# Kernel tuning notes

Measured on AMD Instinct MI355X. Metric: run time of the kernel, lower is better.

Reference implementation:

```python
import jax, jax.numpy as jnp
import numpy as np

S = 7  # output_size
B, C, HF, WF = 8, 256, 160, 160
N = 128
IMG = 640


def setup_inputs() -> dict:
    key = jax.random.key(0)
    k1, k2, k3, k4 = jax.random.split(key, 4)
    feature_map = jax.random.normal(k1, (B, C, HF, WF), jnp.float32)
    # boxes in image-pixel coordinates (the module divides by image_size itself)
    pts = jax.random.uniform(k2, (B, N, 2, 2), jnp.float32, 0.0, float(IMG))
    lo = jnp.min(pts, axis=2)  # (x1, y1)
    hi = jnp.max(pts, axis=2)  # (x2, y2)
    bboxes = jnp.concatenate([lo, hi], axis=-1)  # [B, N, 4]
    proj_w = jax.random.normal(k3, (C, C), jnp.float32) * (1.0 / np.sqrt(C))
    proj_b = jax.random.normal(k4, (C,), jnp.float32) * 0.01
    return {"feature_map": feature_map, "bboxes": bboxes,
            "proj_w": proj_w, "proj_b": proj_b,
            "image_h": IMG, "image_w": IMG}


def _forward(feature_map, bboxes, proj_w, proj_b, image_h, image_w):
    Bb, Cc, Hf, Wf = feature_map.shape
    # 1x1 conv projection
    f = jnp.einsum('bchw,oc->bohw', feature_map, proj_w) + proj_b[None, :, None, None]
    # scale boxes from image coords to feature coords, then integer clip (as in torch code)
    sx = float(Wf) / float(image_w)
    sy = float(Hf) / float(image_h)
    x1 = jnp.clip(jnp.floor(bboxes[..., 0] * sx).astype(jnp.int32), 0, Wf - 1)
    y1 = jnp.clip(jnp.floor(bboxes[..., 1] * sy).astype(jnp.int32), 0, Hf - 1)
    x2 = jnp.clip(jnp.floor(bboxes[..., 2] * sx).astype(jnp.int32), x1 + 1, Wf)
    y2 = jnp.clip(jnp.floor(bboxes[..., 3] * sy).astype(jnp.int32), y1 + 1, Hf)
    Lx = x2 - x1  # [B, N], >= 1 by construction
    Ly = y2 - y1
    i = jnp.arange(S, dtype=jnp.int32)
    # adaptive_avg_pool2d bin edges: start=floor(i*L/S), end=ceil((i+1)*L/S)
    rs = y1[..., None] + (i * Ly[..., None]) // S            # [B, N, S]
    re = y1[..., None] + ((i + 1) * Ly[..., None] + S - 1) // S
    cs = x1[..., None] + (i * Lx[..., None]) // S
    ce = x1[..., None] + ((i + 1) * Lx[..., None] + S - 1) // S
    # summed-area table (zero-padded): I[b,c,y,x] = sum of f[b,c,:y,:x]
    I = jnp.cumsum(jnp.cumsum(f, axis=2), axis=3)
    I = jnp.pad(I, ((0, 0), (0, 0), (1, 0), (1, 0)))

    def per_batch(Ib, rs_b, re_b, cs_b, ce_b):
        # Ib: [C, Hf+1, Wf+1]; index arrays: [N, S]
        tl = Ib[:, rs_b[:, :, None], cs_b[:, None, :]]
        tr = Ib[:, rs_b[:, :, None], ce_b[:, None, :]]
        bl = Ib[:, re_b[:, :, None], cs_b[:, None, :]]
        br = Ib[:, re_b[:, :, None], ce_b[:, None, :]]
        return br - tr - bl + tl  # [C, N, S, S]

    sums = jax.vmap(per_batch)(I, rs, re, cs, ce)  # [B, C, N, S, S]
    counts = ((re - rs)[..., :, None] * (ce - cs)[..., None, :]).astype(f.dtype)  # [B, N, S, S]
    region_features = jnp.transpose(sums, (0, 2, 1, 3, 4)) / counts[:, :, None, :, :]
    # area in raw bbox units, as in the original code
    area_ratios = (bboxes[..., 2] - bboxes[..., 0]) * (bboxes[..., 3] - bboxes[..., 1])
    return region_features, area_ratios


def reference(feature_map, bboxes, proj_w, proj_b, image_h, image_w):
    return _forward(feature_map, bboxes, proj_w, proj_b, image_h, image_w)
```

## Files before the change

### kernel.cpp

```cpp
#include <hip/hip_runtime.h>
#include <hip/hip_bf16.h>

#define BB 8
#define NN 128
#define CC 256
#define HFD 160
#define WFD 160
#define SS 7
#define REGION_OUT_ELEMS (8*128*256*49)

typedef short short8 __attribute__((ext_vector_type(8)));
typedef float f32x4  __attribute__((ext_vector_type(4)));

__global__ __launch_bounds__(256) void k0_convert_w(const float* __restrict__ W,
                                                    __hip_bfloat16* __restrict__ Wb) {
    int o = blockIdx.x;
    int c = threadIdx.x;
    Wb[o * CC + c] = __float2bfloat16(W[o * CC + c]);
}

__global__ __launch_bounds__(256) void k1_rowsum_transpose(const float* __restrict__ fm,
                                                           float* __restrict__ R) {
    int bid = blockIdx.x;
    int cq  = bid & 3;
    int bh  = bid >> 2;
    int h   = bh % HFD;
    int b   = bh / HFD;
    int c0  = cq * 64;
    int t   = threadIdx.x;

    __shared__ float tile[64][161];
    __shared__ float segsum[64][5];

    #pragma unroll
    for (int it = 0; it < 10; ++it) {
        int vid = it * 256 + t;
        int c_l = vid / 40;
        int wq  = vid - c_l * 40;
        f32x4 v = __builtin_nontemporal_load(
            (const f32x4*)(fm + (((size_t)(b * CC + c0 + c_l)) * HFD + h) * WFD + wq * 4));
        tile[c_l][wq * 4 + 0] = v.x;
        tile[c_l][wq * 4 + 1] = v.y;
        tile[c_l][wq * 4 + 2] = v.z;
        tile[c_l][wq * 4 + 3] = v.w;
    }
    __syncthreads();

    int seg = t >> 6;
    int row = t & 63;
    {
        float s = 0.f;
        int w0 = seg * 40;
        #pragma unroll 8
        for (int k = 0; k < 40; ++k) {
            s += tile[row][w0 + k];
            tile[row][w0 + k] = s;
        }
        segsum[row][seg] = s;
    }
    __syncthreads();
    if (t < 64) {
        float a0 = segsum[t][0];
        float a1 = a0 + segsum[t][1];
        float a2 = a1 + segsum[t][2];
        segsum[t][1] = a0;
        segsum[t][2] = a1;
        segsum[t][3] = a2;
    }
    __syncthreads();
    if (seg > 0) {
        float off = segsum[row][seg];
        int w0 = seg * 40;
        #pragma unroll 8
        for (int k = 0; k < 40; ++k) tile[row][w0 + k] += off;
    }
    __syncthreads();

    size_t obase = (((size_t)b * HFD + h) * WFD) * CC + c0;
    #pragma unroll
    for (int it = 0; it < 10; ++it) {
        int vid = it * 256 + t;
        int w   = vid >> 4;
        int cg  = vid & 15;
        float4 o;
        o.x = tile[cg * 4 + 0][w];
        o.y = tile[cg * 4 + 1][w];
        o.z = tile[cg * 4 + 2][w];
        o.w = tile[cg * 4 + 3][w];
        *(float4*)(R + obase + (size_t)w * CC + cg * 4) = o;
    }
}

__global__ __launch_bounds__(256) void k2_colsum(float* __restrict__ I) {
    int w = blockIdx.x % WFD;
    int b = blockIdx.x / WFD;
    int c = threadIdx.x;
    float* p = I + (((size_t)b * HFD) * WFD + w) * CC + c;
    const size_t stride = (size_t)WFD * CC;
    float s = 0.f;
    #pragma unroll 16
    for (int h = 0; h < HFD; ++h) {
        float v = p[(size_t)h * stride];
        s += v;
        p[(size_t)h * stride] = s;
    }
}

__global__ __launch_bounds__(512) void k3a_gather(
        const float* __restrict__ I, const float* __restrict__ bboxes,
        const int* __restrict__ ih_p, const int* __restrict__ iw_p,
        __hip_bfloat16* __restrict__ Pm, float* __restrict__ out) {
    int bn = blockIdx.x;
    int b  = bn >> 7;
    int t  = threadIdx.x;
    int c  = t & 255;
    int half = t >> 8;

    float bx1 = bboxes[bn * 4 + 0];
    float by1 = bboxes[bn * 4 + 1];
    float bx2 = bboxes[bn * 4 + 2];
    float by2 = bboxes[bn * 4 + 3];
    float sx = (float)WFD / (float)iw_p[0];
    float sy = (float)HFD / (float)ih_p[0];

    int x1 = min(max((int)floorf(bx1 * sx), 0), WFD - 1);
    int y1 = min(max((int)floorf(by1 * sy), 0), HFD - 1);
    int x2 = min(max((int)floorf(bx2 * sx), x1 + 1), WFD);
    int y2 = min(max((int)floorf(by2 * sy), y1 + 1), HFD);
    int Lx = x2 - x1, Ly = y2 - y1;

    int rs[SS], re[SS], cs[SS], ce[SS];
    #pragma unroll
    for (int i = 0; i < SS; ++i) {
        rs[i] = y1 + (i * Ly) / SS;
        re[i] = y1 + ((i + 1) * Ly + SS - 1) / SS;
        cs[i] = x1 + (i * Lx) / SS;
        ce[i] = x1 + ((i + 1) * Lx + SS - 1) / SS;
    }

    const size_t Ib = (size_t)b * HFD * WFD * CC;
    __hip_bfloat16* pmb = Pm + (size_t)bn * 64 * CC;

#define GATHER_CELL(cell)                                                        \
    {                                                                            \
        const int i_ = (cell) / SS, j_ = (cell) % SS;                            \
        int r0 = rs[i_] - 1, r1 = re[i_] - 1;                                    \
        int c0 = cs[j_] - 1, c1 = ce[j_] - 1;                                    \
        float br = I[Ib + ((size_t)(r1 * WFD + c1)) * CC + c];                   \
        float tr = (r0 >= 0) ? I[Ib + ((size_t)(r0 * WFD + c1)) * CC + c] : 0.f; \
        float bl = (c0 >= 0) ? I[Ib + ((size_t)(r1 * WFD + c0)) * CC + c] : 0.f; \
        float tl = (r0 >= 0 && c0 >= 0) ? I[Ib + ((size_t)(r0 * WFD + c0)) * CC + c] : 0.f; \
        float cnt = (float)(re[i_] - rs[i_]) * (float)(ce[j_] - cs[j_]);         \
        pmb[(cell) * CC + c] = __float2bfloat16((br - tr - bl + tl) / cnt);      \
    }

    if (half == 0) {
        #pragma unroll
        for (int k = 0; k < 25; ++k) GATHER_CELL(k);
    } else {
        #pragma unroll
        for (int k = 25; k < 49; ++k) GATHER_CELL(k);
        __hip_bfloat16 z = __float2bfloat16(0.f);
        #pragma unroll
        for (int r = 49; r < 64; ++r) pmb[r * CC + c] = z;
    }
#undef GATHER_CELL

    if (t == 0) {
        __builtin_nontemporal_store((bx2 - bx1) * (by2 - by1), &out[REGION_OUT_ELEMS + bn]);
    }
}

__global__ __launch_bounds__(256) void k3b_gemm(
        const __hip_bfloat16* __restrict__ Wb, const __hip_bfloat16* __restrict__ Pm,
        const float* __restrict__ bias, float* __restrict__ out) {
    int bn = blockIdx.x;
    int t  = threadIdx.x;
    const int lane = t & 63;
    const int wv   = t >> 6;
    const int ln   = lane & 15;
    const int quad = lane >> 4;
    const int ob0  = wv * 64;

    const short* A  = (const short*)Wb;
    const short* Bm = (const short*)(Pm + (size_t)bn * 64 * CC);

    f32x4 z = {0.f, 0.f, 0.f, 0.f};
    f32x4 acc[4][4];
    #pragma unroll
    for (int mt = 0; mt < 4; ++mt)
        #pragma unroll
        for (int nt = 0; nt < 4; ++nt) acc[mt][nt] = z;

    #pragma unroll
    for (int k0 = 0; k0 < CC; k0 += 32) {
        short8 a[4], bf[4];
        #pragma unroll
        for (int mt = 0; mt < 4; ++mt)
            a[mt] = *(const short8*)(A + (ob0 + mt * 16 + ln) * CC + k0 + quad * 8);
        #pragma unroll
        for (int nt = 0; nt < 4; ++nt)
            bf[nt] = *(const short8*)(Bm + (nt * 16 + ln) * CC + k0 + quad * 8);
        #pragma unroll
        for (int mt = 0; mt < 4; ++mt)
            #pragma unroll
            for (int nt = 0; nt < 4; ++nt)
                acc[mt][nt] = __builtin_amdgcn_mfma_f32_16x16x32_bf16(a[mt], bf[nt], acc[mt][nt], 0, 0, 0);
    }

    size_t obase = (size_t)bn * CC * 49;
    #pragma unroll
    for (int mt = 0; mt < 4; ++mt) {
        f32x4 bv = *(const f32x4*)(bias + ob0 + mt * 16 + quad * 4);
        #pragma unroll
        for (int nt = 0; nt < 4; ++nt) {
            int cell = nt * 16 + ln;
            if (cell < 49) {
                #pragma unroll
                for (int reg = 0; reg < 4; ++reg) {
                    int o = ob0 + mt * 16 + quad * 4 + reg;
                    __builtin_nontemporal_store(acc[mt][nt][reg] + bv[reg],
                                                &out[obase + (size_t)o * 49 + cell]);
                }
            }
        }
    }
}

extern "C" void kernel_launch(void* const* d_in, const int* in_sizes, int n_in,
                              void* d_out, int out_size, void* d_ws, size_t ws_size,
                              hipStream_t stream) {
    const float* fm     = (const float*)d_in[0];
    const float* bboxes = (const float*)d_in[1];
    const float* W      = (const float*)d_in[2];
    const float* bias   = (const float*)d_in[3];
    const int*   ih     = (const int*)d_in[4];
    const int*   iw     = (const int*)d_in[5];
    float* out = (float*)d_out;

    __hip_bfloat16* Wb = (__hip_bfloat16*)d_ws;
    float* I = (float*)((char*)d_ws + (size_t)CC * CC * 2 + 256);
    I = (float*)(((uintptr_t)I + 1023) & ~(uintptr_t)1023);
    __hip_bfloat16* Pm = (__hip_bfloat16*)((char*)I + (size_t)BB * HFD * WFD * CC * 4);
    Pm = (__hip_bfloat16*)(((uintptr_t)Pm + 1023) & ~(uintptr_t)1023);

    k0_convert_w<<<CC, 256, 0, stream>>>(W, Wb);
    k1_rowsum_transpose<<<BB * HFD * 4, 256, 0, stream>>>(fm, I);
    k2_colsum<<<BB * WFD, 256, 0, stream>>>(I);
    k3a_gather<<<BB * NN, 512, 0, stream>>>(I, bboxes, ih, iw, Pm, out);
    k3b_gemm<<<BB * NN, 256, 0, stream>>>(Wb, Pm, bias, out);
}
```

Measured before the change: 461.5 us.

## Drop column prefix-sum pass and sum row-prefix values per bin in gather

Removes the separate kernel that turned the row-prefix buffer into a full summed-area table. The gather kernel instead iterates over every row of each pooling bin and accumulates right-minus-left differences from the row-prefix sums. This eliminates one full read/write pass over the large intermediate buffer, but gather reads now scale with box height and the gather block is halved to 256 threads.

```diff
diff --git a/kernel.cpp b/kernel.cpp
--- a/kernel.cpp
+++ b/kernel.cpp
@@ -91,30 +91,13 @@
     }
 }
 
-__global__ __launch_bounds__(256) void k2_colsum(float* __restrict__ I) {
-    int w = blockIdx.x % WFD;
-    int b = blockIdx.x / WFD;
-    int c = threadIdx.x;
-    float* p = I + (((size_t)b * HFD) * WFD + w) * CC + c;
-    const size_t stride = (size_t)WFD * CC;
-    float s = 0.f;
-    #pragma unroll 16
-    for (int h = 0; h < HFD; ++h) {
-        float v = p[(size_t)h * stride];
-        s += v;
-        p[(size_t)h * stride] = s;
-    }
-}
-
-__global__ __launch_bounds__(512) void k3a_gather(
-        const float* __restrict__ I, const float* __restrict__ bboxes,
+__global__ __launch_bounds__(256) void k3a_gather(
+        const float* __restrict__ R, const float* __restrict__ bboxes,
         const int* __restrict__ ih_p, const int* __restrict__ iw_p,
         __hip_bfloat16* __restrict__ Pm, float* __restrict__ out) {
     int bn = blockIdx.x;
     int b  = bn >> 7;
-    int t  = threadIdx.x;
-    int c  = t & 255;
-    int half = t >> 8;
+    int c  = threadIdx.x;
 
     float bx1 = bboxes[bn * 4 + 0];
     float by1 = bboxes[bn * 4 + 1];
@@ -129,44 +112,55 @@
     int y2 = min(max((int)floorf(by2 * sy), y1 + 1), HFD);
     int Lx = x2 - x1, Ly = y2 - y1;
 
-    int rs[SS], re[SS], cs[SS], ce[SS];
+    int rs[SS], re[SS], cR[SS], cL[SS];
+    float lm[SS];
+    float cw[SS];
     #pragma unroll
     for (int i = 0; i < SS; ++i) {
         rs[i] = y1 + (i * Ly) / SS;
         re[i] = y1 + ((i + 1) * Ly + SS - 1) / SS;
-        cs[i] = x1 + (i * Lx) / SS;
-        ce[i] = x1 + ((i + 1) * Lx + SS - 1) / SS;
-    }
-
-    const size_t Ib = (size_t)b * HFD * WFD * CC;
+        int cs_ = x1 + (i * Lx) / SS;
+        int ce_ = x1 + ((i + 1) * Lx + SS - 1) / SS;
+        cR[i] = ce_ - 1;
+        cL[i] = (cs_ - 1 >= 0) ? cs_ - 1 : 0;
+        lm[i] = (cs_ - 1 >= 0) ? 1.f : 0.f;
+        cw[i] = (float)(ce_ - cs_);
+    }
+
+    const float* Rb = R + (size_t)b * HFD * WFD * CC + c;
     __hip_bfloat16* pmb = Pm + (size_t)bn * 64 * CC;
 
-#define GATHER_CELL(cell)                                                        \
-    {                                                                            \
-        const int i_ = (cell) / SS, j_ = (cell) % SS;                            \
-        int r0 = rs[i_] - 1, r1 = re[i_] - 1;                                    \
-        int c0 = cs[j_] - 1, c1 = ce[j_] - 1;                                    \
-        float br = I[Ib + ((size_t)(r1 * WFD + c1)) * CC + c];                   \
-        float tr = (r0 >= 0) ? I[Ib + ((size_t)(r0 * WFD + c1)) * CC + c] : 0.f; \
-        float bl = (c0 >= 0) ? I[Ib + ((size_t)(r1 * WFD + c0)) * CC + c] : 0.f; \
-        float tl = (r0 >= 0 && c0 >= 0) ? I[Ib + ((size_t)(r0 * WFD + c0)) * CC + c] : 0.f; \
-        float cnt = (float)(re[i_] - rs[i_]) * (float)(ce[j_] - cs[j_]);         \
-        pmb[(cell) * CC + c] = __float2bfloat16((br - tr - bl + tl) / cnt);      \
-    }
-
-    if (half == 0) {
-        #pragma unroll
-        for (int k = 0; k < 25; ++k) GATHER_CELL(k);
-    } else {
-        #pragma unroll
-        for (int k = 25; k < 49; ++k) GATHER_CELL(k);
+    #pragma unroll
+    for (int i = 0; i < SS; ++i) {
+        float acc[SS];
+        #pragma unroll
+        for (int j = 0; j < SS; ++j) acc[j] = 0.f;
+
+        #pragma unroll 2
+        for (int r = rs[i]; r < re[i]; ++r) {
+            const float* rowp = Rb + (size_t)(r * WFD) * CC;
+            #pragma unroll
+            for (int j = 0; j < SS; ++j) {
+                float right = rowp[cR[j] * CC];
+                float left  = rowp[cL[j] * CC] * lm[j];
+                acc[j] += right - left;
+            }
+        }
+
+        float rh = (float)(re[i] - rs[i]);
+        #pragma unroll
+        for (int j = 0; j < SS; ++j) {
+            pmb[(i * SS + j) * CC + c] = __float2bfloat16(acc[j] / (rh * cw[j]));
+        }
+    }
+
+    {
         __hip_bfloat16 z = __float2bfloat16(0.f);
         #pragma unroll
         for (int r = 49; r < 64; ++r) pmb[r * CC + c] = z;
     }
-#undef GATHER_CELL
-
-    if (t == 0) {
+
+    if (c == 0) {
         __builtin_nontemporal_store((bx2 - bx1) * (by2 - by1), &out[REGION_OUT_ELEMS + bn]);
     }
 }
@@ -239,14 +233,13 @@
     float* out = (float*)d_out;
 
     __hip_bfloat16* Wb = (__hip_bfloat16*)d_ws;
-    float* I = (float*)((char*)d_ws + (size_t)CC * CC * 2 + 256);
-    I = (float*)(((uintptr_t)I + 1023) & ~(uintptr_t)1023);
-    __hip_bfloat16* Pm = (__hip_bfloat16*)((char*)I + (size_t)BB * HFD * WFD * CC * 4);
+    float* R = (float*)((char*)d_ws + (size_t)CC * CC * 2 + 256);
+    R = (float*)(((uintptr_t)R + 1023) & ~(uintptr_t)1023);
+    __hip_bfloat16* Pm = (__hip_bfloat16*)((char*)R + (size_t)BB * HFD * WFD * CC * 4);
     Pm = (__hip_bfloat16*)(((uintptr_t)Pm + 1023) & ~(uintptr_t)1023);
 
     k0_convert_w<<<CC, 256, 0, stream>>>(W, Wb);
-    k1_rowsum_transpose<<<BB * HFD * 4, 256, 0, stream>>>(fm, I);
-    k2_colsum<<<BB * WFD, 256, 0, stream>>>(I);
-    k3a_gather<<<BB * NN, 512, 0, stream>>>(I, bboxes, ih, iw, Pm, out);
+    k1_rowsum_transpose<<<BB * HFD * 4, 256, 0, stream>>>(fm, R);
+    k3a_gather<<<BB * NN, 256, 0, stream>>>(R, bboxes, ih, iw, Pm, out);
     k3b_gemm<<<BB * NN, 256, 0, stream>>>(Wb, Pm, bias, out);
 }
```

New measurement: 482.1 us. +4.5%, slower.
